# Optimization experiments

Measured on AMD Instinct MI355X. Metric: run time of the kernel, lower is better.

The kernel has to match this reference:

```python
import jax, jax.numpy as jnp
import numpy as np

NC, NB, NT = 512, 128, 256   # feats dims: [channels, batch, time]
H = 512                      # hidden_size
NCLS = 97                    # num_classes
NUM_STEPS = 32               # fixed decode length (= text_length.max())


def setup_inputs() -> dict:
    key = jax.random.key(0)
    ks = jax.random.split(key, 12)
    s = 1.0 / np.sqrt(H)
    inp = {
        "feats": jax.random.normal(ks[0], (NC, NB, NT), jnp.float32),
        "text_length": jnp.full((NB,), NUM_STEPS, jnp.int32),
        # AttentionCell params
        "Wi2h": jax.random.normal(ks[1], (H, NC), jnp.float32) * s,   # i2h, no bias
        "Wh2h": jax.random.normal(ks[2], (H, H), jnp.float32) * s,
        "bh2h": jax.random.normal(ks[3], (H,), jnp.float32) * s,
        "Wscore": jax.random.normal(ks[4], (1, H), jnp.float32) * s,  # score, no bias
        # GRUCell params (gate order: r, z, n as in PyTorch)
        "Wih": jax.random.normal(ks[5], (3 * H, NC), jnp.float32) * s,
        "Whh": jax.random.normal(ks[6], (3 * H, H), jnp.float32) * s,
        "bih": jax.random.normal(ks[7], (3 * H,), jnp.float32) * s,
        "bhh": jax.random.normal(ks[8], (3 * H,), jnp.float32) * s,
        # generator: Linear(hidden_size, num_classes - 1)
        "Wgen": jax.random.normal(ks[9], (NCLS - 1, H), jnp.float32) * s,
        "bgen": jax.random.normal(ks[10], (NCLS - 1,), jnp.float32) * s,
    }
    return inp


def reference(feats, text_length, Wi2h, Wh2h, bh2h, Wscore, Wih, Whh, bih, bhh, Wgen, bgen):
    # feats: [nC, nB, nT]
    nC, nB, nT = feats.shape
    # i2h(feats) is step-independent -> hoist out of the loop (same math)
    feats_proj = jnp.einsum('cbt,hc->bth', feats, Wi2h)  # [nB, nT, H]
    w_score = Wscore[0]                                   # [H]

    def step(h, _):
        # additive attention
        hp = h @ Wh2h.T + bh2h                                  # [nB, H]
        e = jnp.tanh(feats_proj + hp[:, None, :]) @ w_score     # [nB, nT]
        alpha = jax.nn.softmax(e, axis=1)                       # [nB, nT]
        context = jnp.einsum('cbt,bt->bc', feats, alpha)        # [nB, nC]
        # GRUCell(context, h), PyTorch semantics
        gi = context @ Wih.T + bih                              # [nB, 3H]
        gh = h @ Whh.T + bhh                                    # [nB, 3H]
        ir, iz, in_ = jnp.split(gi, 3, axis=1)
        hr, hz, hn = jnp.split(gh, 3, axis=1)
        r = jax.nn.sigmoid(ir + hr)
        z = jax.nn.sigmoid(iz + hz)
        n = jnp.tanh(in_ + r * hn)
        h_new = (1.0 - z) * n + z * h
        return h_new, h_new

    h0 = jnp.zeros((nB, feats_proj.shape[-1]), feats.dtype)
    _, hiddens = jax.lax.scan(step, h0, None, length=NUM_STEPS)  # [T, nB, H]
    # all lengths == NUM_STEPS -> gather is a per-batch flatten
    new_hiddens = hiddens.transpose(1, 0, 2).reshape(-1, hiddens.shape[-1])  # [nB*T, H]
    probs = new_hiddens @ Wgen.T + bgen                          # [nB*T, NCLS-1]
    return probs
```

## Files before the change

kernel.cpp:

```cpp
#include <hip/hip_runtime.h>
#include <math.h>

#define NBATCH 128
#define NTIME  256
#define NCH    512
#define NH     512
#define NSTEPS 32
#define NOUT   96
#define MTOT   32768

typedef __attribute__((ext_vector_type(8))) short short8v;
typedef __attribute__((ext_vector_type(4))) float f32x4;

typedef const __attribute__((address_space(1))) unsigned int g_as_uint;
typedef __attribute__((address_space(3))) unsigned int l_as_uint;

__device__ __forceinline__ void gl_lds16(const void* g, void* l) {
    __builtin_amdgcn_global_load_lds((g_as_uint*)g, (l_as_uint*)l, 16, 0, 0);
}

__device__ __forceinline__ float fast_tanh(float x) {
    x = fminf(fmaxf(x, -30.f), 30.f);
    float u = __expf(2.f * x);
    return (u - 1.f) / (u + 1.f);
}
__device__ __forceinline__ float fast_sigmoid(float x) {
    x = fminf(fmaxf(x, -30.f), 30.f);
    return 1.f / (1.f + __expf(-x));
}
__device__ __forceinline__ float wave_reduce_sum(float s) {
    #pragma unroll
    for (int off = 32; off; off >>= 1) s += __shfl_xor(s, off, 64);
    return s;
}
__device__ __forceinline__ float wave_reduce_max(float s) {
    #pragma unroll
    for (int off = 32; off; off >>= 1) s = fmaxf(s, __shfl_xor(s, off, 64));
    return s;
}
__device__ __forceinline__ unsigned short f2bf(float f) {
    unsigned u = __builtin_bit_cast(unsigned, f);
    return (unsigned short)((u + 0x7FFFu + ((u >> 16) & 1u)) >> 16);
}
__device__ __forceinline__ float bflo(unsigned u) {
    return __builtin_bit_cast(float, u << 16);
}
__device__ __forceinline__ float bfhi(unsigned u) {
    return __builtin_bit_cast(float, u & 0xFFFF0000u);
}

__global__ __launch_bounds__(256) void k_w2bf(const float* __restrict__ W,
                                              unsigned short* __restrict__ Wb) {
    #pragma unroll
    for (int r = 0; r < 4; ++r) {
        int idx = (blockIdx.x * 256 + threadIdx.x) + r * 16384;
        float4 v = *(const float4*)(W + (size_t)idx * 4);
        ushort4 o;
        o.x = f2bf(v.x); o.y = f2bf(v.y); o.z = f2bf(v.z); o.w = f2bf(v.w);
        *(ushort4*)(Wb + (size_t)idx * 4) = o;
    }
}

__global__ __launch_bounds__(256) void k_wg2bf(const float* __restrict__ Wih,
                                               const float* __restrict__ Whh,
                                               unsigned short* __restrict__ Wgb) {
    #pragma unroll
    for (int r = 0; r < 4; ++r) {
        int idx = (blockIdx.x * 256 + threadIdx.x) + r * 98304;
        const float* src = (idx < 196608) ? (Wih + (size_t)idx * 4)
                                          : (Whh + (size_t)(idx - 196608) * 4);
        float4 v = *(const float4*)src;
        ushort4 o;
        o.x = f2bf(v.x); o.y = f2bf(v.y); o.z = f2bf(v.z); o.w = f2bf(v.w);
        *(ushort4*)(Wgb + (size_t)idx * 4) = o;
    }
}

__global__ __launch_bounds__(256) void k_prep(const float* __restrict__ feats,
                                              unsigned short* __restrict__ featsb,
                                              unsigned short* __restrict__ Fb) {
    __shared__ float tl[64][65];
    const int m0 = (blockIdx.x & 511) * 64;
    const int k0 = (blockIdx.x >> 9) * 64;
    const int tid = threadIdx.x;
    #pragma unroll
    for (int p = 0; p < 4; ++p) {
        int fid = tid + p * 256;
        int row = fid >> 4, c4 = fid & 15;
        float4 v = *(const float4*)(feats + (size_t)(k0 + row) * MTOT + m0 + c4 * 4);
        tl[row][c4 * 4 + 0] = v.x; tl[row][c4 * 4 + 1] = v.y;
        tl[row][c4 * 4 + 2] = v.z; tl[row][c4 * 4 + 3] = v.w;
        ushort4 o;
        o.x = f2bf(v.x); o.y = f2bf(v.y); o.z = f2bf(v.z); o.w = f2bf(v.w);
        *(ushort4*)(featsb + (size_t)(k0 + row) * MTOT + m0 + c4 * 4) = o;
    }
    __syncthreads();
    #pragma unroll
    for (int p = 0; p < 4; ++p) {
        int cid = tid + p * 256;
        int mm = cid >> 4, ch = cid & 15;
        ushort4 o;
// ... 99 lines not shown
                for (int mf = 0; mf < 8; ++mf)
                    acc[hf][mf] = __builtin_amdgcn_mfma_f32_16x16x32_bf16(
                        a[hf], b[mf], acc[hf][mf], 0, 0, 0);
        }
        __syncthreads();
    }
    #pragma unroll
    for (int hf = 0; hf < 4; ++hf) {
        #pragma unroll
        for (int mf = 0; mf < 8; ++mf) {
            int ml = wm * 128 + mf * 16 + (lane & 15);
            int col = wh * 16 + (lane >> 4) * 4;
            tl[ml * 33 + col + 0] = acc[hf][mf][0];
            tl[ml * 33 + col + 1] = acc[hf][mf][1];
            tl[ml * 33 + col + 2] = acc[hf][mf][2];
            tl[ml * 33 + col + 3] = acc[hf][mf][3];
        }
        __syncthreads();
        #pragma unroll
        for (int mi = 0; mi < 8; ++mi) {
            int ml = (tid >> 3) + mi * 32;
            int hl4 = (tid & 7) * 4;
            float v0 = tl[ml * 33 + hl4 + 0];
            float v1 = tl[ml * 33 + hl4 + 1];
            float v2 = tl[ml * 33 + hl4 + 2];
            float v3 = tl[ml * 33 + hl4 + 3];
            int hg = h0 + ((hl4 < 16) ? (hf * 16 + hl4) : (64 + hf * 16 + hl4 - 16));
            ushort4 o;
            o.x = f2bf(v0); o.y = f2bf(v1); o.z = f2bf(v2); o.w = f2bf(v3);
            *(ushort4*)(fp_bf + (size_t)(m0 + ml) * 512 + hg) = o;
        }
        __syncthreads();
    }
}

__global__ __launch_bounds__(256) void k_wt(const float* __restrict__ W,
                                            unsigned short* __restrict__ WTb) {
    __shared__ float tl[32][33];
    const int bi = blockIdx.x & 15, bj = blockIdx.x >> 4;
    const int tx = threadIdx.x & 31, ty8 = threadIdx.x >> 5;
    #pragma unroll
    for (int i = 0; i < 4; ++i) {
        int r = ty8 * 4 + i;
        tl[r][tx] = W[(size_t)(bj * 32 + r) * NH + bi * 32 + tx];
    }
    __syncthreads();
    #pragma unroll
    for (int i = 0; i < 4; ++i) {
        int c = ty8 * 4 + i;
        WTb[(size_t)(bi * 32 + c) * NH + bj * 32 + tx] = f2bf(tl[tx][c]);
    }
}

__global__ __launch_bounds__(1024) void k_hp0(const float* __restrict__ bh2h,
                                              float* __restrict__ hp) {
    int i = blockIdx.x * 1024 + threadIdx.x;
    hp[i] = bh2h[i & 511];
}

__global__ __launch_bounds__(512) void k_e(const unsigned short* __restrict__ fp_bf,
                                           const float* __restrict__ hp,
                                           const float* __restrict__ wscore,
                                           float* __restrict__ e) {
    const int b = blockIdx.x >> 3;
    const int t0 = (blockIdx.x & 7) * 32;
    const int tid = threadIdx.x;
    const int lane = tid & 63, w = tid >> 6;
    float4 h0 = *(const float4*)(hp + (size_t)b * NH + lane * 8);
    float4 h1 = *(const float4*)(hp + (size_t)b * NH + lane * 8 + 4);
    float4 w0 = *(const float4*)(wscore + lane * 8);
    float4 w1 = *(const float4*)(wscore + lane * 8 + 4);
    const unsigned short* base = fp_bf + (size_t)(b * NTIME + t0 + w * 4) * NH + lane * 8;
    uint4 v0 = *(const uint4*)(base);
    uint4 v1 = *(const uint4*)(base + NH);
    uint4 v2 = *(const uint4*)(base + 2 * NH);
    uint4 v3 = *(const uint4*)(base + 3 * NH);
    uint4 vv[4] = {v0, v1, v2, v3};
    #pragma unroll
    for (int it = 0; it < 4; ++it) {
        uint4 v = vv[it];
        float s = fast_tanh(bflo(v.x) + h0.x) * w0.x + fast_tanh(bfhi(v.x) + h0.y) * w0.y +
                  fast_tanh(bflo(v.y) + h0.z) * w0.z + fast_tanh(bfhi(v.y) + h0.w) * w0.w +
                  fast_tanh(bflo(v.z) + h1.x) * w1.x + fast_tanh(bfhi(v.z) + h1.y) * w1.y +
                  fast_tanh(bflo(v.w) + h1.z) * w1.z + fast_tanh(bfhi(v.w) + h1.w) * w1.w;
        s = wave_reduce_sum(s);
        if (lane == 0) e[b * NTIME + t0 + w * 4 + it] = s;
    }
}

__global__ __launch_bounds__(512) void k_ctx2(const float* __restrict__ e,
                                              const unsigned short* __restrict__ featsb,
                                              unsigned short* __restrict__ ctx_bf) {
    __shared__ float als[256];
    __shared__ float red[8];
    const int b = blockIdx.x >> 3;
    const int c0 = (blockIdx.x & 7) * 64;
    const int tid = threadIdx.x;
    const int lane = tid & 63, w = tid >> 6;
    float v = (tid < 256) ? e[b * NTIME + tid] : -3.4e38f;
    float m = wave_reduce_max(v);
    if (lane == 0) red[w] = m;
    __syncthreads();
    m = red[0];
    #pragma unroll
    for (int i = 1; i < 8; ++i) m = fmaxf(m, red[i]);
    float ex = (tid < 256) ? __expf(v - m) : 0.f;
    float s = wave_reduce_sum(ex);
    __syncthreads();
    if (lane == 0) red[w] = s;
    __syncthreads();
    s = 0.f;
    #pragma unroll
    for (int i = 0; i < 8; ++i) s += red[i];
    if (tid < 256) als[tid] = ex / s;
    __syncthreads();

    float4 al = *(const float4*)&als[lane * 4];
    #pragma unroll
    for (int cc = 0; cc < 8; ++cc) {
        int c = c0 + w * 8 + cc;
        uint2 fv = *(const uint2*)(featsb + (size_t)(c * NBATCH + b) * NTIME + lane * 4);
        float sc = bflo(fv.x) * al.x + bfhi(fv.x) * al.y +
                   bflo(fv.y) * al.z + bfhi(fv.y) * al.w;
        sc = wave_reduce_sum(sc);
        if (lane == 0) ctx_bf[(size_t)b * NCH + c] = f2bf(sc);
    }
}

__global__ __launch_bounds__(256) void k_gmfma(const unsigned short* __restrict__ ctx_bf,
                                               const unsigned short* __restrict__ h_bf,
                                               const unsigned short* __restrict__ Wgb,
                                               float* __restrict__ g2) {
    __shared__ unsigned short As[128 * 64];
    __shared__ unsigned short Bs[128 * 64];
    const int j0 = blockIdx.x * 128;
    const unsigned short* A = (j0 < 1536) ? ctx_bf : h_bf;
    const int tid = threadIdx.x;
    const int lane = tid & 63;
    const int wid = __builtin_amdgcn_readfirstlane(tid >> 6);
    const int wb = wid & 1, wj = wid >> 1;
    const int l8 = lane >> 3, c8 = lane & 7;
    f32x4 acc[4][4];
    #pragma unroll
    for (int i = 0; i < 4; ++i)
        #pragma unroll
        for (int j = 0; j < 4; ++j) acc[i][j] = (f32x4)0.f;

    for (int k0 = 0; k0 < 512; k0 += 64) {
        #pragma unroll
        for (int i = 0; i < 4; ++i) {
            int slot = wid * 4 + i;
            int row = slot * 8 + l8;
            int src_off = (c8 ^ (row & 7)) << 3;
            gl_lds16(A + (size_t)row * 512 + k0 + src_off, As + slot * 512);
            gl_lds16(Wgb + (size_t)(j0 + row) * 512 + k0 + src_off, Bs + slot * 512);
        }
        __syncthreads();
        #pragma unroll
        for (int ks = 0; ks < 2; ++ks) {
            short8v a[4], b[4];
            #pragma unroll
            for (int f = 0; f < 4; ++f) {
                int rowa = wb * 64 + f * 16 + (lane & 15);
                int rowb = wj * 64 + f * 16 + (lane & 15);
                int ch = ks * 4 + (lane >> 4);
                a[f] = *(const short8v*)(As + rowa * 64 + ((ch ^ (rowa & 7)) << 3));
                b[f] = *(const short8v*)(Bs + rowb * 64 + ((ch ^ (rowb & 7)) << 3));
            }
            #pragma unroll
            for (int bf = 0; bf < 4; ++bf)
                #pragma unroll
                for (int jf = 0; jf < 4; ++jf)
                    acc[bf][jf] = __builtin_amdgcn_mfma_f32_16x16x32_bf16(
                        a[bf], b[jf], acc[bf][jf], 0, 0, 0);
        }
        __syncthreads();
    }
    #pragma unroll
    for (int bf = 0; bf < 4; ++bf) {
        int b = wb * 64 + bf * 16 + (lane >> 4) * 4;
        #pragma unroll
        for (int jf = 0; jf < 4; ++jf) {
            int j = j0 + wj * 64 + jf * 16 + (lane & 15);
            *(f32x4*)(g2 + (size_t)j * NBATCH + b) = acc[bf][jf];
        }
    }
}

__global__ __launch_bounds__(1024) void k_comb_hp(const float* __restrict__ g2,
                                                  const float* __restrict__ hprev,
                                                  float* __restrict__ hidn,
                                                  unsigned short* __restrict__ h_bf,
                                                  const float* __restrict__ bih,
                                                  const float* __restrict__ bhh,
                                                  const unsigned short* __restrict__ WTb,
                                                  const float* __restrict__ bh2h,
                                                  float* __restrict__ hp) {
    __shared__ float h_s[4 * 512];
    __shared__ float scr2[16 * 4 * 16 * 4];
    const int blk = blockIdx.x;
    const int b0 = (blk >> 3) * 4;
    const int jbase = (blk & 7) * 64;
    const int tid = threadIdx.x;
    #pragma unroll
    for (int rep = 0; rep < 2; ++rep) {
        int idx = tid + rep * 1024;
        int bi = idx & 3, kk = idx >> 2;
        int b = b0 + bi;
        float ir  = g2[(size_t)(0 * 512 + kk) * NBATCH + b] + bih[kk];
        float iz  = g2[(size_t)(1 * 512 + kk) * NBATCH + b] + bih[512 + kk];
        float in_ = g2[(size_t)(2 * 512 + kk) * NBATCH + b] + bih[1024 + kk];
        float hr  = g2[(size_t)(3 * 512 + kk) * NBATCH + b] + bhh[kk];
        float hz  = g2[(size_t)(4 * 512 + kk) * NBATCH + b] + bhh[512 + kk];
        float hn  = g2[(size_t)(5 * 512 + kk) * NBATCH + b] + bhh[1024 + kk];
        float r = fast_sigmoid(ir + hr);
        float z = fast_sigmoid(iz + hz);
        float ng = fast_tanh(in_ + r * hn);
        float hv = hprev[(size_t)b * NH + kk];
        float hnew = (1.f - z) * ng + z * hv;
        h_s[bi * 512 + kk] = hnew;
        if ((blk & 7) == 0) {
            hidn[(size_t)b * NH + kk] = hnew;
            h_bf[(size_t)b * NH + kk] = f2bf(hnew);
        }
    }
    __syncthreads();
    {
        const int jq = tid & 15, bi = (tid >> 4) & 3, kq = tid >> 6;
        const int j = jbase + jq * 4;
        float4 acc = make_float4(0.f, 0.f, 0.f, 0.f);
        #pragma unroll 8
        for (int kk = 0; kk < 32; ++kk) {
            int k = kq * 32 + kk;
            uint2 wq = *(const uint2*)(WTb + (size_t)k * NH + j);
            float hv = h_s[bi * 512 + k];
            acc.x += hv * bflo(wq.x); acc.y += hv * bfhi(wq.x);
            acc.z += hv * bflo(wq.y); acc.w += hv * bfhi(wq.y);
        }
        *(float4*)&scr2[((kq * 4 + bi) * 16 + jq) * 4] = acc;
    }
    __syncthreads();
    if (tid < 64) {
        const int bi = tid >> 4, jq = tid & 15;
        float4 sum = make_float4(0.f, 0.f, 0.f, 0.f);
        #pragma unroll
        for (int kq = 0; kq < 16; ++kq) {
            float4 p = *(const float4*)&scr2[((kq * 4 + bi) * 16 + jq) * 4];
            sum.x += p.x; sum.y += p.y; sum.z += p.z; sum.w += p.w;
        }
        int j = jbase + jq * 4;
        float4 bb = *(const float4*)(bh2h + j);
        sum.x += bb.x; sum.y += bb.y; sum.z += bb.z; sum.w += bb.w;
        *(float4*)(hp + (size_t)(b0 + bi) * NH + j) = sum;
    }
}

__global__ __launch_bounds__(256) void k_gen(const float* __restrict__ hid,
                                             const float* __restrict__ Wgen,
                                             const float* __restrict__ bgen,
                                             float* __restrict__ out) {
    __shared__ float As[32][36];
    __shared__ float Bs[32][97];
    const int m0 = blockIdx.x * 32;
    const int tid = threadIdx.x;
    const int tx = tid & 31, ty = tid >> 5;
    float acc[4][3] = {};
    for (int k0 = 0; k0 < 512; k0 += 32) {
        {
            int mm = tid >> 3, kq = (tid & 7) << 2;
            int m = m0 + mm, s = m & 31, b = m >> 5;
            float4 v = *(const float4*)(hid + (size_t)(s + 1) * 65536 + b * 512 + k0 + kq);
            *(float4*)(&As[mm][kq]) = v;
        }
        #pragma unroll
        for (int i = 0; i < 3; ++i) {
            int f4 = tid + i * 256;
            int nn = f4 >> 3, kq = (f4 & 7) << 2;
            float4 v = *(const float4*)(Wgen + (size_t)nn * 512 + k0 + kq);
            Bs[kq + 0][nn] = v.x; Bs[kq + 1][nn] = v.y;
            Bs[kq + 2][nn] = v.z; Bs[kq + 3][nn] = v.w;
        }
        __syncthreads();
        #pragma unroll
        for (int kk = 0; kk < 32; ++kk) {
            float bv[3];
            #pragma unroll
            for (int j = 0; j < 3; ++j) bv[j] = Bs[kk][tx * 3 + j];
            #pragma unroll
            for (int i = 0; i < 4; ++i) {
                float a = As[ty * 4 + i][kk];
                #pragma unroll
                for (int j = 0; j < 3; ++j) acc[i][j] += a * bv[j];
            }
        }
        __syncthreads();
    }
    #pragma unroll
    for (int i = 0; i < 4; ++i)
        #pragma unroll
        for (int j = 0; j < 3; ++j)
            out[(size_t)(m0 + ty * 4 + i) * NOUT + tx * 3 + j] = acc[i][j] + bgen[tx * 3 + j];
}

extern "C" void kernel_launch(void* const* d_in, const int* in_sizes, int n_in,
                              void* d_out, int out_size, void* d_ws, size_t ws_size,
                              hipStream_t stream) {
    const float* feats  = (const float*)d_in[0];
    const float* Wi2h   = (const float*)d_in[2];
    const float* Wh2h   = (const float*)d_in[3];
    const float* bh2h   = (const float*)d_in[4];
    const float* Wscore = (const float*)d_in[5];
    const float* Wih    = (const float*)d_in[6];
    const float* Whh    = (const float*)d_in[7];
    const float* bih    = (const float*)d_in[8];
    const float* bhh    = (const float*)d_in[9];
    const float* Wgen   = (const float*)d_in[10];
    const float* bgen   = (const float*)d_in[11];
    float* out = (float*)d_out;

    float* ws  = (float*)d_ws;
    unsigned short* fp_bf  = (unsigned short*)ws;
    float*          hid    = ws + 8388608;
    float*          hpctx  = hid + 2162688;
    unsigned short* ctx_bf = (unsigned short*)(hpctx + 65536);
    unsigned short* h_bf   = (unsigned short*)(hpctx + 65536 + 32768);
    unsigned short* WTb    = (unsigned short*)(hpctx + 65536 + 65536);
    unsigned short* Wgb    = (unsigned short*)(hpctx + 65536 + 65536 + 131072);
    unsigned short* Wb     = (unsigned short*)(hpctx + 65536 + 65536 + 131072 + 786432);
    unsigned short* Fb     = (unsigned short*)(hpctx + 65536 + 65536 + 131072 + 786432 + 131072);
    const size_t base_floats = 8388608 + 2162688 + 65536 + 32768 + 32768 + 131072 + 786432 + 131072 + 8388608;
    const bool big = ws_size >= (base_floats + 8388608) * sizeof(float);
    unsigned short* featsb = big ? (Fb + 16777216) : Fb;

    float* e  = out;
    float* g2 = out;

    hipMemsetAsync(hid, 0, 65536 * sizeof(float), stream);
    hipMemsetAsync(h_bf, 0, 65536 * sizeof(unsigned short), stream);
    k_wt<<<256, 256, 0, stream>>>(Wh2h, WTb);
    k_w2bf<<<64, 256, 0, stream>>>(Wi2h, Wb);
    k_wg2bf<<<384, 256, 0, stream>>>(Wih, Whh, Wgb);
    if (big) {
        k_prep<<<4096, 256, 0, stream>>>(feats, featsb, Fb);
        k_fp_mfma<<<512, 256, 0, stream>>>(Wb, Fb, fp_bf);
    } else {
        k_feats2bf<<<4096, 256, 0, stream>>>(feats, Fb);
        k_fp_mfma<<<512, 256, 0, stream>>>(Wb, Fb, fp_bf);
        k_fcopy<<<4096, 1024, 0, stream>>>(feats, featsb);
    }
    k_hp0<<<64, 1024, 0, stream>>>(bh2h, hpctx);

    for (int s = 0; s < NSTEPS; ++s) {
        const float* h = hid + (size_t)s * 65536;
        float* hn      = hid + (size_t)(s + 1) * 65536;
        k_e<<<1024, 512, 0, stream>>>(fp_bf, hpctx, Wscore, e);
        k_ctx2<<<1024, 512, 0, stream>>>(e, featsb, ctx_bf);
        k_gmfma<<<24, 256, 0, stream>>>(ctx_bf, h_bf, Wgb, g2);
        k_comb_hp<<<256, 1024, 0, stream>>>(g2, h, hn, h_bf, bih, bhh, WTb, bh2h, hpctx);
    }
    k_gen<<<128, 256, 0, stream>>>(hid, Wgen, bgen, out);
}
```

Before: 1.567 ms.

## Fuse per-step recurrent kernels into one persistent kernel with grid barriers

The 128 per-step launches (attention scores, softmax/context, gate GEMM, GRU combine plus h2h projection) are replaced by one persistent 256-block kernel. Phases are separated by a software grid barrier built on an atomic counter, and shared data moves through relaxed agent-scope atomic loads and stores. This removes launch overhead and inter-kernel gaps. In exchange, work is redistributed so each block does more per phase, only 24 blocks do the GEMM, and the kernel relies on all 256 blocks of 1024 threads being co-resident, with relaxed atomics standing in for proper fences.

```diff
diff --git a/kernel.cpp b/kernel.cpp
--- a/kernel.cpp
+++ b/kernel.cpp
@@ -8,6 +8,7 @@
 #define NSTEPS 32
 #define NOUT   96
 #define MTOT   32768
+#define GRID_P 256
 
 typedef __attribute__((ext_vector_type(8))) short short8v;
 typedef __attribute__((ext_vector_type(4))) float f32x4;
@@ -47,6 +48,40 @@
 }
 __device__ __forceinline__ float bfhi(unsigned u) {
     return __builtin_bit_cast(float, u & 0xFFFF0000u);
+}
+
+__device__ __forceinline__ float ld4f(const float* p) {
+    return __hip_atomic_load(p, __ATOMIC_RELAXED, __HIP_MEMORY_SCOPE_AGENT);
+}
+__device__ __forceinline__ void st4f(float* p, float v) {
+    __hip_atomic_store(p, v, __ATOMIC_RELAXED, __HIP_MEMORY_SCOPE_AGENT);
+}
+__device__ __forceinline__ float2 ld8f(const float* p) {
+    unsigned long long u =
+        __hip_atomic_load((const unsigned long long*)p, __ATOMIC_RELAXED, __HIP_MEMORY_SCOPE_AGENT);
+    return __builtin_bit_cast(float2, u);
+}
+__device__ __forceinline__ void st8f(float* p, float x, float y) {
+    float2 v = make_float2(x, y);
+    __hip_atomic_store((unsigned long long*)p, __builtin_bit_cast(unsigned long long, v),
+                       __ATOMIC_RELAXED, __HIP_MEMORY_SCOPE_AGENT);
+}
+__device__ __forceinline__ unsigned long long ld8u(const unsigned short* p) {
+    return __hip_atomic_load((const unsigned long long*)p, __ATOMIC_RELAXED, __HIP_MEMORY_SCOPE_AGENT);
+}
+__device__ __forceinline__ void st2a(unsigned short* p, unsigned short v) {
+    __hip_atomic_store(p, v, __ATOMIC_RELAXED, __HIP_MEMORY_SCOPE_AGENT);
+}
+
+__device__ __forceinline__ void gbar2(int* cnt, int bar) {
+    __syncthreads();
+    if (threadIdx.x == 0) {
+        __hip_atomic_fetch_add(cnt, 1, __ATOMIC_RELAXED, __HIP_MEMORY_SCOPE_AGENT);
+        while (__hip_atomic_load(cnt, __ATOMIC_RELAXED, __HIP_MEMORY_SCOPE_AGENT)
+               < bar * GRID_P)
+            __builtin_amdgcn_s_sleep(1);
+    }
+    __syncthreads();
 }
 
 __global__ __launch_bounds__(256) void k_w2bf(const float* __restrict__ W,
@@ -252,206 +287,232 @@
     }
 }
 
-__global__ __launch_bounds__(1024) void k_hp0(const float* __restrict__ bh2h,
-                                              float* __restrict__ hp) {
-    int i = blockIdx.x * 1024 + threadIdx.x;
-    hp[i] = bh2h[i & 511];
-}
-
-__global__ __launch_bounds__(512) void k_e(const unsigned short* __restrict__ fp_bf,
-                                           const float* __restrict__ hp,
-                                           const float* __restrict__ wscore,
-                                           float* __restrict__ e) {
-    const int b = blockIdx.x >> 3;
-    const int t0 = (blockIdx.x & 7) * 32;
+__global__ __launch_bounds__(1024) void k_loop2(
+    const unsigned short* __restrict__ fp_bf,
+    const unsigned short* __restrict__ featsb,
+    const float* __restrict__ wscore,
+    const unsigned short* __restrict__ Wgb,
+    const float* __restrict__ bih,
+    const float* __restrict__ bhh,
+    const unsigned short* __restrict__ WTb,
+    const float* __restrict__ bh2h,
+    float* hid,
+    float* hp,
+    unsigned short* ctx_bf,
+    unsigned short* h_bf,
+    float* e,
+    float* g2,
+    int* cnt)
+{
+    __shared__ float POOL[24576];
+    const int blk = blockIdx.x;
     const int tid = threadIdx.x;
     const int lane = tid & 63, w = tid >> 6;
-    float4 h0 = *(const float4*)(hp + (size_t)b * NH + lane * 8);
-    float4 h1 = *(const float4*)(hp + (size_t)b * NH + lane * 8 + 4);
-    float4 w0 = *(const float4*)(wscore + lane * 8);
-    float4 w1 = *(const float4*)(wscore + lane * 8 + 4);
-    const unsigned short* base = fp_bf + (size_t)(b * NTIME + t0 + w * 4) * NH + lane * 8;
-    uint4 v0 = *(const uint4*)(base);
-    uint4 v1 = *(const uint4*)(base + NH);
-    uint4 v2 = *(const uint4*)(base + 2 * NH);
-    uint4 v3 = *(const uint4*)(base + 3 * NH);
-    uint4 vv[4] = {v0, v1, v2, v3};
-    #pragma unroll
-    for (int it = 0; it < 4; ++it) {
-        uint4 v = vv[it];
-        float s = fast_tanh(bflo(v.x) + h0.x) * w0.x + fast_tanh(bfhi(v.x) + h0.y) * w0.y +
-                  fast_tanh(bflo(v.y) + h0.z) * w0.z + fast_tanh(bfhi(v.y) + h0.w) * w0.w +
-                  fast_tanh(bflo(v.z) + h1.x) * w1.x + fast_tanh(bfhi(v.z) + h1.y) * w1.y +
-                  fast_tanh(bflo(v.w) + h1.z) * w1.z + fast_tanh(bfhi(v.w) + h1.w) * w1.w;
-        s = wave_reduce_sum(s);
-        if (lane == 0) e[b * NTIME + t0 + w * 4 + it] = s;
-    }
-}
-
-__global__ __launch_bounds__(512) void k_ctx2(const float* __restrict__ e,
-                                              const unsigned short* __restrict__ featsb,
-                                              unsigned short* __restrict__ ctx_bf) {
-    __shared__ float als[256];
-    __shared__ float red[8];
-    const int b = blockIdx.x >> 3;
-    const int c0 = (blockIdx.x & 7) * 64;
-    const int tid = threadIdx.x;
-    const int lane = tid & 63, w = tid >> 6;
-    float v = (tid < 256) ? e[b * NTIME + tid] : -3.4e38f;
-    float m = wave_reduce_max(v);
-    if (lane == 0) red[w] = m;
-    __syncthreads();
-    m = red[0];
-    #pragma unroll
-    for (int i = 1; i < 8; ++i) m = fmaxf(m, red[i]);
-    float ex = (tid < 256) ? __expf(v - m) : 0.f;
-    float s = wave_reduce_sum(ex);
-    __syncthreads();
-    if (lane == 0) red[w] = s;
-    __syncthreads();
-    s = 0.f;
-    #pragma unroll
-    for (int i = 0; i < 8; ++i) s += red[i];
-    if (tid < 256) als[tid] = ex / s;
-    __syncthreads();
-
-    float4 al = *(const float4*)&als[lane * 4];
-    #pragma unroll
-    for (int cc = 0; cc < 8; ++cc) {
-        int c = c0 + w * 8 + cc;
-        uint2 fv = *(const uint2*)(featsb + (size_t)(c * NBATCH + b) * NTIME + lane * 4);
-        float sc = bflo(fv.x) * al.x + bfhi(fv.x) * al.y +
-                   bflo(fv.y) * al.z + bfhi(fv.y) * al.w;
-        sc = wave_reduce_sum(sc);
-        if (lane == 0) ctx_bf[(size_t)b * NCH + c] = f2bf(sc);
-    }
-}
-
-__global__ __launch_bounds__(256) void k_gmfma(const unsigned short* __restrict__ ctx_bf,
-                                               const unsigned short* __restrict__ h_bf,
-                                               const unsigned short* __restrict__ Wgb,
-                                               float* __restrict__ g2) {
-    __shared__ unsigned short As[128 * 64];
-    __shared__ unsigned short Bs[128 * 64];
-    const int j0 = blockIdx.x * 128;
-    const unsigned short* A = (j0 < 1536) ? ctx_bf : h_bf;
-    const int tid = threadIdx.x;
-    const int lane = tid & 63;
-    const int wid = __builtin_amdgcn_readfirstlane(tid >> 6);
-    const int wb = wid & 1, wj = wid >> 1;
-    const int l8 = lane >> 3, c8 = lane & 7;
-    f32x4 acc[4][4];
-    #pragma unroll
-    for (int i = 0; i < 4; ++i)
-        #pragma unroll
-        for (int j = 0; j < 4; ++j) acc[i][j] = (f32x4)0.f;
-
-    for (int k0 = 0; k0 < 512; k0 += 64) {
-        #pragma unroll
-        for (int i = 0; i < 4; ++i) {
-            int slot = wid * 4 + i;
-            int row = slot * 8 + l8;
-            int src_off = (c8 ^ (row & 7)) << 3;
-            gl_lds16(A + (size_t)row * 512 + k0 + src_off, As + slot * 512);
-            gl_lds16(Wgb + (size_t)(j0 + row) * 512 + k0 + src_off, Bs + slot * 512);
-        }
-        __syncthreads();
-        #pragma unroll
-        for (int ks = 0; ks < 2; ++ks) {
-            short8v a[4], b[4];
-            #pragma unroll
-            for (int f = 0; f < 4; ++f) {
-                int rowa = wb * 64 + f * 16 + (lane & 15);
-                int rowb = wj * 64 + f * 16 + (lane & 15);
-                int ch = ks * 4 + (lane >> 4);
-                a[f] = *(const short8v*)(As + rowa * 64 + ((ch ^ (rowa & 7)) << 3));
-                b[f] = *(const short8v*)(Bs + rowb * 64 + ((ch ^ (rowb & 7)) << 3));
-            }
-            #pragma unroll
-            for (int bf = 0; bf < 4; ++bf)
+    int bar = 0;
+
+    {
+        int idx = blk * 256 + tid;
+        if (idx < 65536) {
+            st4f(hp + idx, bh2h[idx & 511]);
+            st4f(hid + idx, 0.f);
+            st2a(h_bf + idx, (unsigned short)0);
+        }
+    }
+    gbar2(cnt, ++bar);
+
+    for (int s = 0; s < NSTEPS; ++s) {
+        const float* hprev = hid + (size_t)s * 65536;
+        float* hnext      = hid + (size_t)(s + 1) * 65536;
+
+        {
+            const int b = blk >> 1;
+            const int tbase = (blk & 1) * 128 + w * 8;
+            const float* hpb = hp + (size_t)b * NH + lane * 8;
+            float2 ha = ld8f(hpb), hb = ld8f(hpb + 2), hc = ld8f(hpb + 4), hd = ld8f(hpb + 6);
+            float4 w0 = *(const float4*)(wscore + lane * 8);
+            float4 w1 = *(const float4*)(wscore + lane * 8 + 4);
+            #pragma unroll
+            for (int it = 0; it < 8; ++it) {
+                int t = tbase + it;
+                uint4 v = *(const uint4*)(fp_bf + (size_t)(b * NTIME + t) * NH + lane * 8);
+                float sv =
+                    fast_tanh(bflo(v.x) + ha.x) * w0.x + fast_tanh(bfhi(v.x) + ha.y) * w0.y +
+                    fast_tanh(bflo(v.y) + hb.x) * w0.z + fast_tanh(bfhi(v.y) + hb.y) * w0.w +
+                    fast_tanh(bflo(v.z) + hc.x) * w1.x + fast_tanh(bfhi(v.z) + hc.y) * w1.y +
+                    fast_tanh(bflo(v.w) + hd.x) * w1.z + fast_tanh(bfhi(v.w) + hd.y) * w1.w;
+                sv = wave_reduce_sum(sv);
+                if (lane == 0) st4f(e + b * NTIME + t, sv);
+            }
+        }
+        gbar2(cnt, ++bar);
+
+        {
+            float* als = POOL;
+            float* red = POOL + 256;
+            const int b = blk >> 1;
+            const int c0 = (blk & 1) * 256;
+            float v = (tid < 256) ? ld4f(e + b * NTIME + tid) : -3.4e38f;
+            float m = wave_reduce_max(v);
+            if (lane == 0) red[w] = m;
+            __syncthreads();
+            m = red[0];
+            #pragma unroll
+            for (int i = 1; i < 16; ++i) m = fmaxf(m, red[i]);
+            float ex = (tid < 256) ? __expf(v - m) : 0.f;
+            float sm = wave_reduce_sum(ex);
+            __syncthreads();
+            if (lane == 0) red[w] = sm;
+            __syncthreads();
+            sm = 0.f;
+            #pragma unroll
+            for (int i = 0; i < 16; ++i) sm += red[i];
+            __syncthreads();
+            if (tid < 256) als[tid] = ex / sm;
+            __syncthreads();
+            float4 al = *(const float4*)&als[lane * 4];
+            #pragma unroll
+            for (int cc = 0; cc < 16; ++cc) {
+                int c = c0 + w * 16 + cc;
+                uint2 fv = *(const uint2*)(featsb + (size_t)(c * NBATCH + b) * NTIME + lane * 4);
+                float sc = bflo(fv.x) * al.x + bfhi(fv.x) * al.y +
+                           bflo(fv.y) * al.z + bfhi(fv.y) * al.w;
+                sc = wave_reduce_sum(sc);
+                if (lane == 0) st2a(ctx_bf + (size_t)b * NCH + c, f2bf(sc));
+            }
+        }
+        gbar2(cnt, ++bar);
+
+        {
+            const bool blkact = (blk < 24);
+            const bool act = blkact && (tid < 256);
+            const int j0 = blk * 128;
+            const unsigned short* Aact = (j0 < 1536) ? ctx_bf : h_bf;
+            unsigned short* AsU = (unsigned short*)POOL;
+            unsigned short* BsU = AsU + 8192;
+            const int wid4 = tid >> 6;
+            const int wb = wid4 & 1, wj = wid4 >> 1;
+            const int l8 = lane >> 3, c8 = lane & 7;
+            f32x4 acc[4][4];
+            #pragma unroll
+            for (int i = 0; i < 4; ++i)
                 #pragma unroll
-                for (int jf = 0; jf < 4; ++jf)
-                    acc[bf][jf] = __builtin_amdgcn_mfma_f32_16x16x32_bf16(
-                        a[bf], b[jf], acc[bf][jf], 0, 0, 0);
-        }
-        __syncthreads();
-    }
-    #pragma unroll
-    for (int bf = 0; bf < 4; ++bf) {
-        int b = wb * 64 + bf * 16 + (lane >> 4) * 4;
-        #pragma unroll
-        for (int jf = 0; jf < 4; ++jf) {
-            int j = j0 + wj * 64 + jf * 16 + (lane & 15);
-            *(f32x4*)(g2 + (size_t)j * NBATCH + b) = acc[bf][jf];
-        }
-    }
-}
-
-__global__ __launch_bounds__(1024) void k_comb_hp(const float* __restrict__ g2,
-                                                  const float* __restrict__ hprev,
-                                                  float* __restrict__ hidn,
-                                                  unsigned short* __restrict__ h_bf,
-                                                  const float* __restrict__ bih,
-                                                  const float* __restrict__ bhh,
-                                                  const unsigned short* __restrict__ WTb,
-                                                  const float* __restrict__ bh2h,
-                                                  float* __restrict__ hp) {
-    __shared__ float h_s[4 * 512];
-    __shared__ float scr2[16 * 4 * 16 * 4];
-    const int blk = blockIdx.x;
-    const int b0 = (blk >> 3) * 4;
-    const int jbase = (blk & 7) * 64;
-    const int tid = threadIdx.x;
-    #pragma unroll
-    for (int rep = 0; rep < 2; ++rep) {
-        int idx = tid + rep * 1024;
-        int bi = idx & 3, kk = idx >> 2;
-        int b = b0 + bi;
-        float ir  = g2[(size_t)(0 * 512 + kk) * NBATCH + b] + bih[kk];
-        float iz  = g2[(size_t)(1 * 512 + kk) * NBATCH + b] + bih[512 + kk];
-        float in_ = g2[(size_t)(2 * 512 + kk) * NBATCH + b] + bih[1024 + kk];
-        float hr  = g2[(size_t)(3 * 512 + kk) * NBATCH + b] + bhh[kk];
-        float hz  = g2[(size_t)(4 * 512 + kk) * NBATCH + b] + bhh[512 + kk];
-        float hn  = g2[(size_t)(5 * 512 + kk) * NBATCH + b] + bhh[1024 + kk];
-        float r = fast_sigmoid(ir + hr);
-        float z = fast_sigmoid(iz + hz);
-        float ng = fast_tanh(in_ + r * hn);
-        float hv = hprev[(size_t)b * NH + kk];
-        float hnew = (1.f - z) * ng + z * hv;
-        h_s[bi * 512 + kk] = hnew;
-        if ((blk & 7) == 0) {
-            hidn[(size_t)b * NH + kk] = hnew;
-            h_bf[(size_t)b * NH + kk] = f2bf(hnew);
-        }
-    }
-    __syncthreads();
-    {
-        const int jq = tid & 15, bi = (tid >> 4) & 3, kq = tid >> 6;
-        const int j = jbase + jq * 4;
-        float4 acc = make_float4(0.f, 0.f, 0.f, 0.f);
-        #pragma unroll 8
-        for (int kk = 0; kk < 32; ++kk) {
-            int k = kq * 32 + kk;
-            uint2 wq = *(const uint2*)(WTb + (size_t)k * NH + j);
-            float hv = h_s[bi * 512 + k];
-            acc.x += hv * bflo(wq.x); acc.y += hv * bfhi(wq.x);
-            acc.z += hv * bflo(wq.y); acc.w += hv * bfhi(wq.y);
-        }
-        *(float4*)&scr2[((kq * 4 + bi) * 16 + jq) * 4] = acc;
-    }
-    __syncthreads();
-    if (tid < 64) {
-        const int bi = tid >> 4, jq = tid & 15;
-        float4 sum = make_float4(0.f, 0.f, 0.f, 0.f);
-        #pragma unroll
-        for (int kq = 0; kq < 16; ++kq) {
-            float4 p = *(const float4*)&scr2[((kq * 4 + bi) * 16 + jq) * 4];
-            sum.x += p.x; sum.y += p.y; sum.z += p.z; sum.w += p.w;
-        }
-        int j = jbase + jq * 4;
-        float4 bb = *(const float4*)(bh2h + j);
-        sum.x += bb.x; sum.y += bb.y; sum.z += bb.z; sum.w += bb.w;
-        *(float4*)(hp + (size_t)(b0 + bi) * NH + j) = sum;
+                for (int j = 0; j < 4; ++j) acc[i][j] = (f32x4)0.f;
+
+            for (int k0 = 0; k0 < 512; k0 += 64) {
+                if (act) {
+                    #pragma unroll
+                    for (int i = 0; i < 4; ++i) {
+                        int cid = tid + i * 256;
+                        int row = cid >> 3, ch = cid & 7;
+                        const unsigned short* src = Aact + (size_t)row * 512 + k0 + ch * 8;
+                        unsigned long long lo = ld8u(src);
+                        unsigned long long hi = ld8u(src + 4);
+                        unsigned short* dst = AsU + row * 64 + ((ch ^ (row & 7)) << 3);
+                        *(unsigned long long*)(dst)     = lo;
+                        *(unsigned long long*)(dst + 4) = hi;
+                        int slot = wid4 * 4 + i;
+                        int rowb = slot * 8 + l8;
+                        gl_lds16(Wgb + (size_t)(j0 + rowb) * 512 + k0 + ((c8 ^ (rowb & 7)) << 3),
+                                 BsU + slot * 512);
+                    }
+                }
+                __syncthreads();
+                if (act) {
+                    #pragma unroll
+                    for (int ks = 0; ks < 2; ++ks) {
+                        short8v a[4], b[4];
+                        #pragma unroll
+                        for (int f = 0; f < 4; ++f) {
+                            int rowa = wb * 64 + f * 16 + (lane & 15);
+                            int rowb = wj * 64 + f * 16 + (lane & 15);
+                            int ch = ks * 4 + (lane >> 4);
+                            a[f] = *(const short8v*)(AsU + rowa * 64 + ((ch ^ (rowa & 7)) << 3));
+                            b[f] = *(const short8v*)(BsU + rowb * 64 + ((ch ^ (rowb & 7)) << 3));
+                        }
+                        #pragma unroll
+                        for (int bf = 0; bf < 4; ++bf)
+                            #pragma unroll
+                            for (int jf = 0; jf < 4; ++jf)
+                                acc[bf][jf] = __builtin_amdgcn_mfma_f32_16x16x32_bf16(
+                                    a[bf], b[jf], acc[bf][jf], 0, 0, 0);
+                    }
+                }
+                __syncthreads();
+            }
+            if (act) {
+                #pragma unroll
+                for (int bf = 0; bf < 4; ++bf) {
+                    int b = wb * 64 + bf * 16 + (lane >> 4) * 4;
+                    #pragma unroll
+                    for (int jf = 0; jf < 4; ++jf) {
+                        int j = j0 + wj * 64 + jf * 16 + (lane & 15);
+                        st8f(g2 + (size_t)j * NBATCH + b,     acc[bf][jf][0], acc[bf][jf][1]);
+                        st8f(g2 + (size_t)j * NBATCH + b + 2, acc[bf][jf][2], acc[bf][jf][3]);
+                    }
+                }
+            }
+        }
+        gbar2(cnt, ++bar);
+
+        {
+            float* h_s  = POOL;
+            float* scr2 = POOL + 2048;
+            const int b0 = (blk >> 3) * 4;
+            const int jbase = (blk & 7) * 64;
+            #pragma unroll
+            for (int rep = 0; rep < 2; ++rep) {
+                int idx = tid + rep * 1024;
+                int bi = idx & 3, kk = idx >> 2;
+                int b = b0 + bi;
+                float ir  = ld4f(g2 + (size_t)(0 * 512 + kk) * NBATCH + b) + bih[kk];
+                float iz  = ld4f(g2 + (size_t)(1 * 512 + kk) * NBATCH + b) + bih[512 + kk];
+                float in_ = ld4f(g2 + (size_t)(2 * 512 + kk) * NBATCH + b) + bih[1024 + kk];
+                float hr  = ld4f(g2 + (size_t)(3 * 512 + kk) * NBATCH + b) + bhh[kk];
+                float hz  = ld4f(g2 + (size_t)(4 * 512 + kk) * NBATCH + b) + bhh[512 + kk];
+                float hn  = ld4f(g2 + (size_t)(5 * 512 + kk) * NBATCH + b) + bhh[1024 + kk];
+                float r = fast_sigmoid(ir + hr);
+                float z = fast_sigmoid(iz + hz);
+                float ng = fast_tanh(in_ + r * hn);
+                float hv = ld4f(hprev + (size_t)b * NH + kk);
+                float hnew = (1.f - z) * ng + z * hv;
+                h_s[bi * 512 + kk] = hnew;
+                if ((blk & 7) == 0) {
+                    st4f(hnext + (size_t)b * NH + kk, hnew);
+                    st2a(h_bf + (size_t)b * NH + kk, f2bf(hnew));
+                }
+            }
+            __syncthreads();
+            {
+                const int jq = tid & 15, bi = (tid >> 4) & 3, kq = tid >> 6;
+                const int j = jbase + jq * 4;
+                float4 acc4 = make_float4(0.f, 0.f, 0.f, 0.f);
+                #pragma unroll 8
+                for (int kk = 0; kk < 32; ++kk) {
+                    int k = kq * 32 + kk;
+                    uint2 wq = *(const uint2*)(WTb + (size_t)k * NH + j);
+                    float hv = h_s[bi * 512 + k];
+                    acc4.x += hv * bflo(wq.x); acc4.y += hv * bfhi(wq.x);
+                    acc4.z += hv * bflo(wq.y); acc4.w += hv * bfhi(wq.y);
+                }
+                *(float4*)&scr2[((kq * 4 + bi) * 16 + jq) * 4] = acc4;
+            }
+            __syncthreads();
+            if (tid < 64) {
+                const int bi = tid >> 4, jq = tid & 15;
+                float4 sum = make_float4(0.f, 0.f, 0.f, 0.f);
+                #pragma unroll
+                for (int kq = 0; kq < 16; ++kq) {
+                    float4 p = *(const float4*)&scr2[((kq * 4 + bi) * 16 + jq) * 4];
+                    sum.x += p.x; sum.y += p.y; sum.z += p.z; sum.w += p.w;
+                }
+                int j = jbase + jq * 4;
+                float4 bb = *(const float4*)(bh2h + j);
+                st8f(hp + (size_t)(b0 + bi) * NH + j,     sum.x + bb.x, sum.y + bb.y);
+                st8f(hp + (size_t)(b0 + bi) * NH + j + 2, sum.z + bb.z, sum.w + bb.w);
+            }
+            __syncthreads();
+        }
+        if (s < NSTEPS - 1) gbar2(cnt, ++bar);
     }
 }
 
@@ -521,22 +582,23 @@
     float* ws  = (float*)d_ws;
     unsigned short* fp_bf  = (unsigned short*)ws;
     float*          hid    = ws + 8388608;
-    float*          hpctx  = hid + 2162688;
-    unsigned short* ctx_bf = (unsigned short*)(hpctx + 65536);
-    unsigned short* h_bf   = (unsigned short*)(hpctx + 65536 + 32768);
-    unsigned short* WTb    = (unsigned short*)(hpctx + 65536 + 65536);
-    unsigned short* Wgb    = (unsigned short*)(hpctx + 65536 + 65536 + 131072);
-    unsigned short* Wb     = (unsigned short*)(hpctx + 65536 + 65536 + 131072 + 786432);
-    unsigned short* Fb     = (unsigned short*)(hpctx + 65536 + 65536 + 131072 + 786432 + 131072);
-    const size_t base_floats = 8388608 + 2162688 + 65536 + 32768 + 32768 + 131072 + 786432 + 131072 + 8388608;
+    float*          hp     = hid + 2162688;
+    unsigned short* ctx_bf = (unsigned short*)(hp + 65536);
+    unsigned short* h_bf   = (unsigned short*)(hp + 65536 + 32768);
+    unsigned short* WTb    = (unsigned short*)(hp + 65536 + 65536);
+    unsigned short* Wgb    = (unsigned short*)(hp + 65536 + 65536 + 131072);
+    unsigned short* Wb     = (unsigned short*)(hp + 65536 + 65536 + 131072 + 786432);
+    int*            cnt    = (int*)(hp + 65536 + 65536 + 131072 + 786432 + 131072);
+    unsigned short* Fb     = (unsigned short*)(hp + 65536 + 65536 + 131072 + 786432 + 131072 + 16);
+    const size_t base_floats = 8388608 + 2162688 + 65536 + 32768 + 32768 + 131072
+                             + 786432 + 131072 + 16 + 8388608;
     const bool big = ws_size >= (base_floats + 8388608) * sizeof(float);
     unsigned short* featsb = big ? (Fb + 16777216) : Fb;
 
     float* e  = out;
     float* g2 = out;
 
-    hipMemsetAsync(hid, 0, 65536 * sizeof(float), stream);
-    hipMemsetAsync(h_bf, 0, 65536 * sizeof(unsigned short), stream);
+    hipMemsetAsync(cnt, 0, 16, stream);
     k_wt<<<256, 256, 0, stream>>>(Wh2h, WTb);
     k_w2bf<<<64, 256, 0, stream>>>(Wi2h, Wb);
     k_wg2bf<<<384, 256, 0, stream>>>(Wih, Whh, Wgb);
@@ -548,15 +610,10 @@
         k_fp_mfma<<<512, 256, 0, stream>>>(Wb, Fb, fp_bf);
         k_fcopy<<<4096, 1024, 0, stream>>>(feats, featsb);
     }
-    k_hp0<<<64, 1024, 0, stream>>>(bh2h, hpctx);
-
-    for (int s = 0; s < NSTEPS; ++s) {
-        const float* h = hid + (size_t)s * 65536;
-        float* hn      = hid + (size_t)(s + 1) * 65536;
-        k_e<<<1024, 512, 0, stream>>>(fp_bf, hpctx, Wscore, e);
-        k_ctx2<<<1024, 512, 0, stream>>>(e, featsb, ctx_bf);
-        k_gmfma<<<24, 256, 0, stream>>>(ctx_bf, h_bf, Wgb, g2);
-        k_comb_hp<<<256, 1024, 0, stream>>>(g2, h, hn, h_bf, bih, bhh, WTb, bh2h, hpctx);
-    }
+
+    k_loop2<<<GRID_P, 1024, 0, stream>>>(fp_bf, featsb, Wscore, Wgb, bih, bhh,
+                                         WTb, bh2h, hid, hp, ctx_bf, h_bf,
+                                         e, g2, cnt);
+
     k_gen<<<128, 256, 0, stream>>>(hid, Wgen, bgen, out);
 }
```

New measurement: 4.476 ms. +185.6%, slower.

## Fuse attention score and context into one kernel using a fixed softmax shift

Applied to the files above, without the earlier changes.

Merges the score kernel and the softmax/context kernel into a single kernel per step. Because |e| is bounded by sum|wscore|, it uses that bound as a fixed shift instead of a max reduction, then accumulates the unnormalized context and the exp-sum with atomics. Normalization is deferred to the GRU combine step, where the context projection is scaled by 1/esum. This removes one launch and the round trip of e through global memory per step. The cost is float atomics, which make the result non-deterministic, plus the fp32-to-bf16 conversion of the context moving into the GEMM's A-tile load, and possible underflow if the bound is loose.

```diff
diff --git a/kernel.cpp b/kernel.cpp
--- a/kernel.cpp
+++ b/kernel.cpp
@@ -33,14 +33,12 @@
     for (int off = 32; off; off >>= 1) s += __shfl_xor(s, off, 64);
     return s;
 }
-__device__ __forceinline__ float wave_reduce_max(float s) {
-    #pragma unroll
-    for (int off = 32; off; off >>= 1) s = fmaxf(s, __shfl_xor(s, off, 64));
-    return s;
-}
 __device__ __forceinline__ unsigned short f2bf(float f) {
     unsigned u = __builtin_bit_cast(unsigned, f);
     return (unsigned short)((u + 0x7FFFu + ((u >> 16) & 1u)) >> 16);
+}
+__device__ __forceinline__ unsigned pk2bf(float a, float b) {
+    return (unsigned)f2bf(a) | ((unsigned)f2bf(b) << 16);
 }
 __device__ __forceinline__ float bflo(unsigned u) {
     return __builtin_bit_cast(float, u << 16);
@@ -252,94 +250,112 @@
     }
 }
 
-__global__ __launch_bounds__(1024) void k_hp0(const float* __restrict__ bh2h,
-                                              float* __restrict__ hp) {
-    int i = blockIdx.x * 1024 + threadIdx.x;
-    hp[i] = bh2h[i & 511];
-}
-
-__global__ __launch_bounds__(512) void k_e(const unsigned short* __restrict__ fp_bf,
-                                           const float* __restrict__ hp,
-                                           const float* __restrict__ wscore,
-                                           float* __restrict__ e) {
+__global__ __launch_bounds__(1024) void k_init(const float* __restrict__ bh2h,
+                                               const float* __restrict__ wscore,
+                                               float* __restrict__ hp,
+                                               float* __restrict__ ctx_un,
+                                               float* __restrict__ esum,
+                                               float* __restrict__ Cbuf) {
+    __shared__ float cred[16];
+    int idx = blockIdx.x * 1024 + threadIdx.x;
+    hp[idx] = bh2h[idx & 511];
+    ctx_un[idx] = 0.f;
+    ctx_un[idx + 65536] = 0.f;
+    if (idx < 256) esum[idx] = 0.f;
+    if (blockIdx.x == 0) {
+        const int tid = threadIdx.x, lane = tid & 63, w = tid >> 6;
+        float v = (tid < 512) ? fabsf(wscore[tid]) : 0.f;
+        v = wave_reduce_sum(v);
+        if (lane == 0) cred[w] = v;
+        __syncthreads();
+        if (tid == 0) {
+            float c = 0.f;
+            #pragma unroll
+            for (int i = 0; i < 16; ++i) c += cred[i];
+            Cbuf[0] = c;
+        }
+    }
+}
+
+__global__ __launch_bounds__(512) void k_ectx(const unsigned short* __restrict__ fp_bf,
+                                              const unsigned short* __restrict__ featsb,
+                                              const float* __restrict__ hp,
+                                              const float* __restrict__ wscore,
+                                              const float* __restrict__ Cbuf,
+                                              float* __restrict__ ctx_un,
+                                              float* __restrict__ esum) {
+    __shared__ float e_s[32];
     const int b = blockIdx.x >> 3;
     const int t0 = (blockIdx.x & 7) * 32;
     const int tid = threadIdx.x;
     const int lane = tid & 63, w = tid >> 6;
-    float4 h0 = *(const float4*)(hp + (size_t)b * NH + lane * 8);
-    float4 h1 = *(const float4*)(hp + (size_t)b * NH + lane * 8 + 4);
-    float4 w0 = *(const float4*)(wscore + lane * 8);
-    float4 w1 = *(const float4*)(wscore + lane * 8 + 4);
-    const unsigned short* base = fp_bf + (size_t)(b * NTIME + t0 + w * 4) * NH + lane * 8;
-    uint4 v0 = *(const uint4*)(base);
-    uint4 v1 = *(const uint4*)(base + NH);
-    uint4 v2 = *(const uint4*)(base + 2 * NH);
-    uint4 v3 = *(const uint4*)(base + 3 * NH);
-    uint4 vv[4] = {v0, v1, v2, v3};
-    #pragma unroll
-    for (int it = 0; it < 4; ++it) {
-        uint4 v = vv[it];
-        float s = fast_tanh(bflo(v.x) + h0.x) * w0.x + fast_tanh(bfhi(v.x) + h0.y) * w0.y +
-                  fast_tanh(bflo(v.y) + h0.z) * w0.z + fast_tanh(bfhi(v.y) + h0.w) * w0.w +
-                  fast_tanh(bflo(v.z) + h1.x) * w1.x + fast_tanh(bfhi(v.z) + h1.y) * w1.y +
-                  fast_tanh(bflo(v.w) + h1.z) * w1.z + fast_tanh(bfhi(v.w) + h1.w) * w1.w;
-        s = wave_reduce_sum(s);
-        if (lane == 0) e[b * NTIME + t0 + w * 4 + it] = s;
-    }
-}
-
-__global__ __launch_bounds__(512) void k_ctx2(const float* __restrict__ e,
-                                              const unsigned short* __restrict__ featsb,
-                                              unsigned short* __restrict__ ctx_bf) {
-    __shared__ float als[256];
-    __shared__ float red[8];
-    const int b = blockIdx.x >> 3;
-    const int c0 = (blockIdx.x & 7) * 64;
-    const int tid = threadIdx.x;
-    const int lane = tid & 63, w = tid >> 6;
-    float v = (tid < 256) ? e[b * NTIME + tid] : -3.4e38f;
-    float m = wave_reduce_max(v);
-    if (lane == 0) red[w] = m;
+    const float C = Cbuf[0];
+
+    {
+        float4 h0 = *(const float4*)(hp + (size_t)b * NH + lane * 8);
+        float4 h1 = *(const float4*)(hp + (size_t)b * NH + lane * 8 + 4);
+        float4 w0 = *(const float4*)(wscore + lane * 8);
+        float4 w1 = *(const float4*)(wscore + lane * 8 + 4);
+        const unsigned short* base = fp_bf + (size_t)(b * NTIME + t0 + w * 4) * NH + lane * 8;
+        uint4 v0 = *(const uint4*)(base);
+        uint4 v1 = *(const uint4*)(base + NH);
+        uint4 v2 = *(const uint4*)(base + 2 * NH);
+        uint4 v3 = *(const uint4*)(base + 3 * NH);
+        uint4 vv[4] = {v0, v1, v2, v3};
+        #pragma unroll
+        for (int it = 0; it < 4; ++it) {
+            uint4 v = vv[it];
+            float sv =
+                fast_tanh(bflo(v.x) + h0.x) * w0.x + fast_tanh(bfhi(v.x) + h0.y) * w0.y +
+                fast_tanh(bflo(v.y) + h0.z) * w0.z + fast_tanh(bfhi(v.y) + h0.w) * w0.w +
+                fast_tanh(bflo(v.z) + h1.x) * w1.x + fast_tanh(bfhi(v.z) + h1.y) * w1.y +
+                fast_tanh(bflo(v.w) + h1.z) * w1.z + fast_tanh(bfhi(v.w) + h1.w) * w1.w;
+            sv = wave_reduce_sum(sv);
+            if (lane == 0) e_s[w * 4 + it] = __expf(sv - C);
+        }
+    }
     __syncthreads();
-    m = red[0];
-    #pragma unroll
-    for (int i = 1; i < 8; ++i) m = fmaxf(m, red[i]);
-    float ex = (tid < 256) ? __expf(v - m) : 0.f;
-    float s = wave_reduce_sum(ex);
-    __syncthreads();
-    if (lane == 0) red[w] = s;
-    __syncthreads();
-    s = 0.f;
-    #pragma unroll
-    for (int i = 0; i < 8; ++i) s += red[i];
-    if (tid < 256) als[tid] = ex / s;
-    __syncthreads();
-
-    float4 al = *(const float4*)&als[lane * 4];
-    #pragma unroll
-    for (int cc = 0; cc < 8; ++cc) {
-        int c = c0 + w * 8 + cc;
-        uint2 fv = *(const uint2*)(featsb + (size_t)(c * NBATCH + b) * NTIME + lane * 4);
-        float sc = bflo(fv.x) * al.x + bfhi(fv.x) * al.y +
-                   bflo(fv.y) * al.z + bfhi(fv.y) * al.w;
-        sc = wave_reduce_sum(sc);
-        if (lane == 0) ctx_bf[(size_t)b * NCH + c] = f2bf(sc);
-    }
-}
-
-__global__ __launch_bounds__(256) void k_gmfma(const unsigned short* __restrict__ ctx_bf,
+
+    if (tid < 64) {
+        float v = (lane < 32) ? e_s[lane] : 0.f;
+        v = wave_reduce_sum(v);
+        if (lane == 0) atomicAdd(esum + b, v);
+    }
+
+    float er[32];
+    #pragma unroll
+    for (int i = 0; i < 8; ++i) {
+        float4 q = *(const float4*)&e_s[i * 4];
+        er[i * 4 + 0] = q.x; er[i * 4 + 1] = q.y;
+        er[i * 4 + 2] = q.z; er[i * 4 + 3] = q.w;
+    }
+    const unsigned short* fb = featsb + ((size_t)tid * NBATCH + b) * NTIME + t0;
+    float acc = 0.f;
+    #pragma unroll
+    for (int q4 = 0; q4 < 4; ++q4) {
+        uint4 fv = *(const uint4*)(fb + q4 * 8);
+        acc += bflo(fv.x) * er[q4 * 8 + 0] + bfhi(fv.x) * er[q4 * 8 + 1]
+             + bflo(fv.y) * er[q4 * 8 + 2] + bfhi(fv.y) * er[q4 * 8 + 3]
+             + bflo(fv.z) * er[q4 * 8 + 4] + bfhi(fv.z) * er[q4 * 8 + 5]
+             + bflo(fv.w) * er[q4 * 8 + 6] + bfhi(fv.w) * er[q4 * 8 + 7];
+    }
+    atomicAdd(ctx_un + (size_t)b * NCH + tid, acc);
+}
+
+__global__ __launch_bounds__(256) void k_gmfma(const float* __restrict__ ctx_un,
                                                const unsigned short* __restrict__ h_bf,
                                                const unsigned short* __restrict__ Wgb,
                                                float* __restrict__ g2) {
     __shared__ unsigned short As[128 * 64];
     __shared__ unsigned short Bs[128 * 64];
     const int j0 = blockIdx.x * 128;
-    const unsigned short* A = (j0 < 1536) ? ctx_bf : h_bf;
+    const bool ctxp = (j0 < 1536);
     const int tid = threadIdx.x;
     const int lane = tid & 63;
     const int wid = __builtin_amdgcn_readfirstlane(tid >> 6);
     const int wb = wid & 1, wj = wid >> 1;
     const int l8 = lane >> 3, c8 = lane & 7;
+    const int arow = tid & 127, ahalf = tid >> 7;
     f32x4 acc[4][4];
     #pragma unroll
     for (int i = 0; i < 4; ++i)
@@ -351,9 +367,29 @@
         for (int i = 0; i < 4; ++i) {
             int slot = wid * 4 + i;
             int row = slot * 8 + l8;
-            int src_off = (c8 ^ (row & 7)) << 3;
-            gl_lds16(A + (size_t)row * 512 + k0 + src_off, As + slot * 512);
-            gl_lds16(Wgb + (size_t)(j0 + row) * 512 + k0 + src_off, Bs + slot * 512);
+            gl_lds16(Wgb + (size_t)(j0 + row) * 512 + k0 + ((c8 ^ (row & 7)) << 3),
+                     Bs + slot * 512);
+        }
+        if (ctxp) {
+            #pragma unroll
+            for (int i = 0; i < 4; ++i) {
+                int ch = ahalf * 4 + i;
+                const float* src = ctx_un + (size_t)arow * 512 + k0 + ch * 8;
+                float4 a0 = *(const float4*)(src);
+                float4 a1 = *(const float4*)(src + 4);
+                uint4 o;
+                o.x = pk2bf(a0.x, a0.y); o.y = pk2bf(a0.z, a0.w);
+                o.z = pk2bf(a1.x, a1.y); o.w = pk2bf(a1.z, a1.w);
+                *(uint4*)(As + arow * 64 + ((ch ^ (arow & 7)) << 3)) = o;
+            }
+        } else {
+            #pragma unroll
+            for (int i = 0; i < 4; ++i) {
+                int slot = wid * 4 + i;
+                int row = slot * 8 + l8;
+                gl_lds16(h_bf + (size_t)row * 512 + k0 + ((c8 ^ (row & 7)) << 3),
+                         As + slot * 512);
+            }
         }
         __syncthreads();
         #pragma unroll
@@ -395,7 +431,10 @@
                                                   const float* __restrict__ bhh,
                                                   const unsigned short* __restrict__ WTb,
                                                   const float* __restrict__ bh2h,
-                                                  float* __restrict__ hp) {
+                                                  float* __restrict__ hp,
+                                                  const float* __restrict__ esum_cur,
+                                                  float* __restrict__ ctx_next,
+                                                  float* __restrict__ esum_next) {
     __shared__ float h_s[4 * 512];
     __shared__ float scr2[16 * 4 * 16 * 4];
     const int blk = blockIdx.x;
@@ -407,9 +446,10 @@
         int idx = tid + rep * 1024;
         int bi = idx & 3, kk = idx >> 2;
         int b = b0 + bi;
-        float ir  = g2[(size_t)(0 * 512 + kk) * NBATCH + b] + bih[kk];
-        float iz  = g2[(size_t)(1 * 512 + kk) * NBATCH + b] + bih[512 + kk];
-        float in_ = g2[(size_t)(2 * 512 + kk) * NBATCH + b] + bih[1024 + kk];
+        float inv = 1.f / esum_cur[b];
+        float ir  = g2[(size_t)(0 * 512 + kk) * NBATCH + b] * inv + bih[kk];
+        float iz  = g2[(size_t)(1 * 512 + kk) * NBATCH + b] * inv + bih[512 + kk];
+        float in_ = g2[(size_t)(2 * 512 + kk) * NBATCH + b] * inv + bih[1024 + kk];
         float hr  = g2[(size_t)(3 * 512 + kk) * NBATCH + b] + bhh[kk];
         float hz  = g2[(size_t)(4 * 512 + kk) * NBATCH + b] + bhh[512 + kk];
         float hn  = g2[(size_t)(5 * 512 + kk) * NBATCH + b] + bhh[1024 + kk];
@@ -452,6 +492,11 @@
         float4 bb = *(const float4*)(bh2h + j);
         sum.x += bb.x; sum.y += bb.y; sum.z += bb.z; sum.w += bb.w;
         *(float4*)(hp + (size_t)(b0 + bi) * NH + j) = sum;
+    }
+    {
+        int idx = blk * 1024 + tid;
+        if (idx < 65536) ctx_next[idx] = 0.f;
+        if (idx < 128)   esum_next[idx] = 0.f;
     }
 }
 
@@ -518,21 +563,23 @@
     const float* bgen   = (const float*)d_in[11];
     float* out = (float*)d_out;
 
-    float* ws  = (float*)d_ws;
-    unsigned short* fp_bf  = (unsigned short*)ws;
-    float*          hid    = ws + 8388608;
-    float*          hpctx  = hid + 2162688;
-    unsigned short* ctx_bf = (unsigned short*)(hpctx + 65536);
-    unsigned short* h_bf   = (unsigned short*)(hpctx + 65536 + 32768);
-    unsigned short* WTb    = (unsigned short*)(hpctx + 65536 + 65536);
-    unsigned short* Wgb    = (unsigned short*)(hpctx + 65536 + 65536 + 131072);
-    unsigned short* Wb     = (unsigned short*)(hpctx + 65536 + 65536 + 131072 + 786432);
-    unsigned short* Fb     = (unsigned short*)(hpctx + 65536 + 65536 + 131072 + 786432 + 131072);
-    const size_t base_floats = 8388608 + 2162688 + 65536 + 32768 + 32768 + 131072 + 786432 + 131072 + 8388608;
+    float* ws = (float*)d_ws;
+    unsigned short* fp_bf = (unsigned short*)ws;
+    float* hid    = ws + 8388608;
+    float* hp     = hid + 2162688;
+    float* ctx_un = hp + 65536;
+    float* esum   = ctx_un + 131072;
+    float* Cbuf   = esum + 256;
+    unsigned short* h_bf = (unsigned short*)(Cbuf + 16);
+    unsigned short* WTb  = (unsigned short*)(Cbuf + 16 + 32768);
+    unsigned short* Wgb  = (unsigned short*)(Cbuf + 16 + 32768 + 131072);
+    unsigned short* Wb   = (unsigned short*)(Cbuf + 16 + 32768 + 131072 + 786432);
+    unsigned short* Fb   = (unsigned short*)(Cbuf + 16 + 32768 + 131072 + 786432 + 131072);
+    const size_t base_floats = 8388608 + 2162688 + 65536 + 131072 + 256 + 16
+                             + 32768 + 131072 + 786432 + 131072 + 8388608;
     const bool big = ws_size >= (base_floats + 8388608) * sizeof(float);
     unsigned short* featsb = big ? (Fb + 16777216) : Fb;
 
-    float* e  = out;
     float* g2 = out;
 
     hipMemsetAsync(hid, 0, 65536 * sizeof(float), stream);
@@ -548,15 +595,19 @@
         k_fp_mfma<<<512, 256, 0, stream>>>(Wb, Fb, fp_bf);
         k_fcopy<<<4096, 1024, 0, stream>>>(feats, featsb);
     }
-    k_hp0<<<64, 1024, 0, stream>>>(bh2h, hpctx);
+    k_init<<<64, 1024, 0, stream>>>(bh2h, Wscore, hp, ctx_un, esum, Cbuf);
 
     for (int s = 0; s < NSTEPS; ++s) {
         const float* h = hid + (size_t)s * 65536;
         float* hn      = hid + (size_t)(s + 1) * 65536;
-        k_e<<<1024, 512, 0, stream>>>(fp_bf, hpctx, Wscore, e);
-        k_ctx2<<<1024, 512, 0, stream>>>(e, featsb, ctx_bf);
-        k_gmfma<<<24, 256, 0, stream>>>(ctx_bf, h_bf, Wgb, g2);
-        k_comb_hp<<<256, 1024, 0, stream>>>(g2, h, hn, h_bf, bih, bhh, WTb, bh2h, hpctx);
+        float* ctxc = ctx_un + (size_t)(s & 1) * 65536;
+        float* esc  = esum + (size_t)(s & 1) * 128;
+        float* ctxn = ctx_un + (size_t)((s + 1) & 1) * 65536;
+        float* esn  = esum + (size_t)((s + 1) & 1) * 128;
+        k_ectx<<<1024, 512, 0, stream>>>(fp_bf, featsb, hp, Wscore, Cbuf, ctxc, esc);
+        k_gmfma<<<24, 256, 0, stream>>>(ctxc, h_bf, Wgb, g2);
+        k_comb_hp<<<256, 1024, 0, stream>>>(g2, h, hn, h_bf, bih, bhh, WTb, bh2h,
+                                            hp, esc, ctxn, esn);
     }
     k_gen<<<128, 256, 0, stream>>>(hid, Wgen, bgen, out);
 }
```

Result: slower. 1.791 ms (+14.3%).
